# Kernel tuning notes

Hardware: AMD Instinct MI355X
Metric: run time of the kernel (lower is better)

## Reference

```python
import jax, jax.numpy as jnp
import numpy as np

B, T, N = 32, 128, 30
D_T, D_V, D_I = 512, 512, 512


def setup_inputs() -> dict:
    key = jax.random.key(0)
    ks = jax.random.split(key, 9)
    return {
        "h_s": jax.random.normal(ks[0], (B, N, D_T), dtype=jnp.float32),
        "h_v": jax.random.normal(ks[1], (B, T, D_V), dtype=jnp.float32),
        "lengths": jax.random.randint(ks[2], (B,), 1, N + 1, dtype=jnp.int32),
        "W_S": jax.random.normal(ks[3], (D_T, D_I), dtype=jnp.float32) * 0.05,
        "b_S": jax.random.normal(ks[4], (D_I,), dtype=jnp.float32) * 0.05,
        "W_V": jax.random.normal(ks[5], (D_V, D_I), dtype=jnp.float32) * 0.05,
        "b_V": jax.random.normal(ks[6], (D_I,), dtype=jnp.float32) * 0.05,
        "W_w": jax.random.normal(ks[7], (D_I,), dtype=jnp.float32) * 0.05,
        "b_w": jax.random.normal(ks[8], (1,), dtype=jnp.float32) * 0.05,
    }


def reference(h_s, h_v, lengths, W_S, b_S, W_V, b_V, W_w, b_w):
    n_tok = h_s.shape[1]
    # token mask (B, N): 1 where position < length
    mask = (lengths[:, None] >= jnp.arange(1, n_tok + 1)[None, :]).astype(h_s.dtype)
    # loop-invariant projections computed once (the torch loop recomputes per t)
    S = h_s @ W_S + b_S                      # (B, N, D_I)
    V = h_v @ W_V + b_V                      # (B, T, D_I)
    # additive attention scores beta: (B, T, N)
    e = jnp.tanh(S[:, None, :, :] + V[:, :, None, :])  # (B, T, N, D_I)
    beta = jnp.einsum('btnd,d->btn', e, W_w) + b_w[0]
    # masked softmax (non-memory-efficient variant, faithful to source)
    m = mask[:, None, :]                      # (B, 1, N)
    p = jax.nn.softmax(beta * m, axis=-1) * m
    alpha = p / (p.sum(axis=-1, keepdims=True) + 1e-13) + 1e-13  # (B, T, N)
    # attended textual features: (B, T, D_T)
    return jnp.einsum('btn,bnd->btd', alpha, h_s)
```

## Files before the change

kernel.cpp:

```cpp
#include <hip/hip_runtime.h>
#include <math.h>

#define BB 32
#define TT 128
#define NTOK 30
#define DD 512
#define C2F 2.885390081777927f

typedef unsigned short ushortT;
typedef __attribute__((ext_vector_type(8))) short bf16x8;
typedef __attribute__((ext_vector_type(4))) float f32x4;

__device__ __forceinline__ ushortT f2bf(float f) {
    unsigned u = __builtin_bit_cast(unsigned, f);
    u += 0x7fffu + ((u >> 16) & 1u);
    return (ushortT)(u >> 16);
}

__device__ __forceinline__ void load_lds16(const ushortT* g, ushortT* l) {
    __builtin_amdgcn_global_load_lds(
        (const __attribute__((address_space(1))) unsigned int*)g,
        (__attribute__((address_space(3))) unsigned int*)l,
        16, 0, 0);
}

#define NCONV ((BB*NTOK*DD + BB*TT*DD)/4/256)
__global__ __launch_bounds__(256) void prep(
    const float* __restrict__ h_s, const float* __restrict__ h_v,
    const float* __restrict__ W_S, const float* __restrict__ W_V,
    ushortT* __restrict__ Abf_s, ushortT* __restrict__ Abf_v,
    ushortT* __restrict__ WtS, ushortT* __restrict__ WtV)
{
    __shared__ ushortT tile[32][33];
    int bx = blockIdx.x;
    if (bx < NCONV) {
        int i = bx * 256 + threadIdx.x;
        const int n0_4 = BB * NTOK * DD / 4;
        const float* x; ushortT* y;
        if (i < n0_4) { x = h_s; y = Abf_s; }
        else { i -= n0_4; x = h_v; y = Abf_v; }
        float4 v = ((const float4*)x)[i];
        ushort4 o;
        o.x = f2bf(v.x); o.y = f2bf(v.y); o.z = f2bf(v.z); o.w = f2bf(v.w);
        ((ushort4*)y)[i] = o;
        return;
    }
    int idx = bx - NCONV;
    const float* W = (idx & 256) ? W_V : W_S;
    ushortT*    T  = (idx & 256) ? WtV : WtS;
    idx &= 255;
    int k0 = (idx >> 4) * 32, n0 = (idx & 15) * 32;
    int c = threadIdx.x & 31, r8 = threadIdx.x >> 5;
    #pragma unroll
    for (int q = 0; q < 4; ++q) {
        int k = r8 + q * 8;
        tile[k][c] = f2bf(W[(size_t)(k0 + k) * DD + n0 + c]);
    }
    __syncthreads();
    #pragma unroll
    for (int q = 0; q < 4; ++q) {
        int n = r8 + q * 8;
        T[(size_t)(n0 + n) * DD + k0 + c] = tile[c][n];
    }
}

__global__ __launch_bounds__(256) void gemm_mfma(
    const ushortT* __restrict__ Abf_s, const ushortT* __restrict__ Abf_v,
    const ushortT* __restrict__ WtS, const ushortT* __restrict__ WtV,
    const float* __restrict__ b_S, const float* __restrict__ b_V,
    float* __restrict__ Sbuf, float* __restrict__ Vbuf)
{
    __shared__ ushortT ldsA[64 * 64];
    __shared__ ushortT ldsB[64 * 64];
    const ushortT* A; const ushortT* Bt; const float* bias; float* Y; int bm;
    if (blockIdx.x < 15) { A = Abf_s; Bt = WtS; bias = b_S; Y = Sbuf; bm = blockIdx.x * 64; }
    else                 { A = Abf_v; Bt = WtV; bias = b_V; Y = Vbuf; bm = (blockIdx.x - 15) * 64; }

    const int tid  = threadIdx.x;
    const int lane = tid & 63;
    const int wid  = tid >> 6;
    const int wr = wid >> 1, wc = wid & 1;
    const int bn = blockIdx.y * 64;

    const int idx0 = tid,       row0 = idx0 >> 3, ch0 = (idx0 & 7) ^ (row0 & 7);
    const int idx1 = 256 + tid, row1 = idx1 >> 3, ch1 = (idx1 & 7) ^ (row1 & 7);
    const ushortT* gA0 = A  + (size_t)(bm + row0) * DD + ch0 * 8;
    const ushortT* gA1 = A  + (size_t)(bm + row1) * DD + ch1 * 8;
    const ushortT* gB0 = Bt + (size_t)(bn + row0) * DD + ch0 * 8;
    const ushortT* gB1 = Bt + (size_t)(bn + row1) * DD + ch1 * 8;
    ushortT* lA0 = ldsA + wid * 512;
    ushortT* lA1 = ldsA + 2048 + wid * 512;
    ushortT* lB0 = ldsB + wid * 512;
    ushortT* lB1 = ldsB + 2048 + wid * 512;

    const int arow = wr * 32 + (lane & 15);
    const int brow = wc * 32 + (lane & 15);
    const int kq   = lane >> 4;
    const int sw   = lane & 7;

    f32x4 acc[2][2];
    #pragma unroll
    for (int i = 0; i < 2; ++i)
        #pragma unroll
        for (int j = 0; j < 2; ++j)
            acc[i][j] = (f32x4){0.f, 0.f, 0.f, 0.f};

    for (int k0 = 0; k0 < DD; k0 += 64) {
        __syncthreads();
        load_lds16(gA0 + k0, lA0);
        load_lds16(gA1 + k0, lA1);
        load_lds16(gB0 + k0, lB0);
        load_lds16(gB1 + k0, lB1);
        __syncthreads();

        bf16x8 af[2][2], bfr[2][2];
        #pragma unroll
        for (int i = 0; i < 2; ++i)
            #pragma unroll
            for (int s = 0; s < 2; ++s) {
                int ra = arow + i * 16;
                af[i][s]  = *(const bf16x8*)(ldsA + ra * 64 + ((s * 4 + kq) ^ sw) * 8);
                int rb = brow + i * 16;
                bfr[i][s] = *(const bf16x8*)(ldsB + rb * 64 + ((s * 4 + kq) ^ sw) * 8);
            }
        #pragma unroll
        for (int s = 0; s < 2; ++s)
            #pragma unroll
            for (int i = 0; i < 2; ++i)
                #pragma unroll
                for (int j = 0; j < 2; ++j)
                    acc[i][j] = __builtin_amdgcn_mfma_f32_16x16x32_bf16(
                        af[i][s], bfr[j][s], acc[i][j], 0, 0, 0);
    }

    #pragma unroll
    for (int i = 0; i < 2; ++i)
        #pragma unroll
        for (int j = 0; j < 2; ++j) {
            int r = bm + wr * 32 + i * 16 + (lane >> 4) * 4;
            int c = bn + wc * 32 + j * 16 + (lane & 15);
            float bv = bias[c];
            #pragma unroll
            for (int reg = 0; reg < 4; ++reg)
                Y[(size_t)(r + reg) * DD + c] = (acc[i][j][reg] + bv) * C2F;
        }
}

__global__ __launch_bounds__(512) void attend2(
    const float* __restrict__ Sbuf, const float* __restrict__ Vbuf,
    const float* __restrict__ h_s, const int* __restrict__ lengths,
    const float* __restrict__ W_w, const float* __restrict__ b_w,
    float* __restrict__ out)
{
    __shared__ float Slds[NTOK * DD];
    const int b  = blockIdx.x >> 3;
    const int tc = blockIdx.x & 7;
    const int tid = threadIdx.x;
    const int t  = tid >> 5;
    const int dg = tid & 31;
    const int t_glob = tc * 16 + t;
    const int len = lengths[b];
    const float bwv = b_w[0];

    const float4* sSrc = (const float4*)(Sbuf + (size_t)b * NTOK * DD);
    float4* sDst = (float4*)Slds;
    #pragma unroll
    for (int i = 0; i < 8; ++i) {
        int idx = i * 512 + tid;
        if (idx < NTOK * DD / 4) sDst[idx] = sSrc[idx];
    }

    const float* Vrow = Vbuf + ((size_t)(b * TT + t_glob)) * DD;
    float4 v4[4], w4[4];
    #pragma unroll
    for (int c = 0; c < 4; ++c) {
        v4[c] = *(const float4*)&Vrow[dg * 4 + 128 * c];
        w4[c] = *(const float4*)&W_w[dg * 4 + 128 * c];
    }
    float wsum = 0.f;
    #pragma unroll
    for (int c = 0; c < 4; ++c) wsum += w4[c].x + w4[c].y + w4[c].z + w4[c].w;

    __syncthreads();

    float pacc[NTOK];
    #pragma unroll
    for (int n = 0; n < NTOK; ++n) {
        const float* Sr = Slds + n * DD;
        float a = 0.f;
        #pragma unroll
        for (int c = 0; c < 4; ++c) {
            float4 s4 = *(const float4*)&Sr[dg * 4 + 128 * c];
            a = fmaf(w4[c].x, __builtin_amdgcn_rcpf(1.f + __builtin_amdgcn_exp2f(s4.x + v4[c].x)), a);
            a = fmaf(w4[c].y, __builtin_amdgcn_rcpf(1.f + __builtin_amdgcn_exp2f(s4.y + v4[c].y)), a);
            a = fmaf(w4[c].z, __builtin_amdgcn_rcpf(1.f + __builtin_amdgcn_exp2f(s4.z + v4[c].z)), a);
            a = fmaf(w4[c].w, __builtin_amdgcn_rcpf(1.f + __builtin_amdgcn_exp2f(s4.w + v4[c].w)), a);
        }
        pacc[n] = a;
    }
    __syncthreads();

    #pragma unroll
    for (int off = 1; off <= 16; off <<= 1) {
        wsum += __shfl_xor(wsum, off, 64);
        #pragma unroll
        for (int n = 0; n < NTOK; ++n) pacc[n] += __shfl_xor(pacc[n], off, 64);
    }

    float mx = -1e30f;
    #pragma unroll
    for (int n = 0; n < NTOK; ++n) {
        float bn = wsum + bwv - 2.f * pacc[n];
        pacc[n] = bn;
        if (n < len) mx = fmaxf(mx, bn);
    }
    float ssum = 0.f;
    #pragma unroll
    for (int n = 0; n < NTOK; ++n) {
        float e = (n < len) ? __expf(pacc[n] - mx) : 0.f;
        pacc[n] = e;
        ssum += e;
    }
    const float inv = 1.f / (ssum + 1e-13f);
    #pragma unroll
    for (int n = 0; n < NTOK; ++n) pacc[n] = pacc[n] * inv + 1e-13f;

    const float4* hSrc = (const float4*)(h_s + (size_t)b * NTOK * DD);
    #pragma unroll
    for (int i = 0; i < 8; ++i) {
        int idx = i * 512 + tid;
        if (idx < NTOK * DD / 4) sDst[idx] = hSrc[idx];
    }
    __syncthreads();

    float4 acc[4];
    #pragma unroll
    for (int c = 0; c < 4; ++c) acc[c] = make_float4(0.f, 0.f, 0.f, 0.f);
    #pragma unroll
    for (int n = 0; n < NTOK; ++n) {
        float a = pacc[n];
        #pragma unroll
        for (int c = 0; c < 4; ++c) {
            float4 h = *(const float4*)&Slds[n * DD + dg * 4 + 128 * c];
            acc[c].x = fmaf(a, h.x, acc[c].x);
            acc[c].y = fmaf(a, h.y, acc[c].y);
            acc[c].z = fmaf(a, h.z, acc[c].z);
            acc[c].w = fmaf(a, h.w, acc[c].w);
        }
    }
    float* Or = out + ((size_t)(b * TT + t_glob)) * DD;
    #pragma unroll
    for (int c = 0; c < 4; ++c)
        *(float4*)&Or[dg * 4 + 128 * c] = acc[c];
}

extern "C" void kernel_launch(void* const* d_in, const int* in_sizes, int n_in,
                              void* d_out, int out_size, void* d_ws, size_t ws_size,
                              hipStream_t stream) {
    const float* h_s     = (const float*)d_in[0];
    const float* h_v     = (const float*)d_in[1];
    const int*   lengths = (const int*)  d_in[2];
    const float* W_S     = (const float*)d_in[3];
    const float* b_S     = (const float*)d_in[4];
    const float* W_V     = (const float*)d_in[5];
    const float* b_V     = (const float*)d_in[6];
    const float* W_w     = (const float*)d_in[7];
    const float* b_w     = (const float*)d_in[8];
    float* out = (float*)d_out;

    float*   Sbuf  = (float*)d_ws;
    float*   Vbuf  = Sbuf + (size_t)BB * NTOK * DD;
    ushortT* Abf_s = (ushortT*)(Vbuf + (size_t)BB * TT * DD);
    ushortT* Abf_v = Abf_s + (size_t)BB * NTOK * DD;
    ushortT* WtS   = Abf_v + (size_t)BB * TT * DD;
    ushortT* WtV   = WtS + (size_t)DD * DD;

    prep<<<NCONV + 512, 256, 0, stream>>>(h_s, h_v, W_S, W_V, Abf_s, Abf_v, WtS, WtV);
    gemm_mfma<<<dim3(15 + 64, DD / 64), 256, 0, stream>>>(
        Abf_s, Abf_v, WtS, WtV, b_S, b_V, Sbuf, Vbuf);
    attend2<<<BB * 8, 512, 0, stream>>>(Sbuf, Vbuf, h_s, lengths, W_w, b_w, out);
}
```

Baseline: 44.17 us.

## Fuse activation bf16 conversion into GEMM and store projections in bf16

```diff
diff --git a/kernel.cpp b/kernel.cpp
--- a/kernel.cpp
+++ b/kernel.cpp
@@ -7,47 +7,50 @@
 #define DD 512
 #define C2F 2.885390081777927f
 
-typedef unsigned short ushortT;
+typedef unsigned short u16;
 typedef __attribute__((ext_vector_type(8))) short bf16x8;
+typedef __attribute__((ext_vector_type(8))) unsigned short u16x8;
 typedef __attribute__((ext_vector_type(4))) float f32x4;
 
-__device__ __forceinline__ ushortT f2bf(float f) {
+__device__ __forceinline__ u16 f2bf(float f) {
     unsigned u = __builtin_bit_cast(unsigned, f);
     u += 0x7fffu + ((u >> 16) & 1u);
-    return (ushortT)(u >> 16);
-}
-
-__device__ __forceinline__ void load_lds16(const ushortT* g, ushortT* l) {
+    return (u16)(u >> 16);
+}
+__device__ __forceinline__ float bf2f(u16 u) {
+    return __builtin_bit_cast(float, (unsigned)u << 16);
+}
+
+__device__ __forceinline__ void load_lds16(const u16* g, u16* l) {
     __builtin_amdgcn_global_load_lds(
         (const __attribute__((address_space(1))) unsigned int*)g,
         (__attribute__((address_space(3))) unsigned int*)l,
         16, 0, 0);
 }
 
-#define NCONV ((BB*NTOK*DD + BB*TT*DD)/4/256)
+template<int CTRL>
+__device__ __forceinline__ float dpp_add(float x) {
+    int yi = __builtin_amdgcn_update_dpp(0, __builtin_bit_cast(int, x), CTRL, 0xF, 0xF, true);
+    return x + __builtin_bit_cast(float, yi);
+}
+__device__ __forceinline__ float red64(float x) {
+    x = dpp_add<0xB1>(x);
+    x = dpp_add<0x4E>(x);
+    x = dpp_add<0x141>(x);
+    x = dpp_add<0x140>(x);
+    x += __shfl_xor(x, 16, 64);
+    x += __shfl_xor(x, 32, 64);
+    return x;
+}
+
 __global__ __launch_bounds__(256) void prep(
-    const float* __restrict__ h_s, const float* __restrict__ h_v,
     const float* __restrict__ W_S, const float* __restrict__ W_V,
-    ushortT* __restrict__ Abf_s, ushortT* __restrict__ Abf_v,
-    ushortT* __restrict__ WtS, ushortT* __restrict__ WtV)
+    u16* __restrict__ WtS, u16* __restrict__ WtV)
 {
-    __shared__ ushortT tile[32][33];
-    int bx = blockIdx.x;
-    if (bx < NCONV) {
-        int i = bx * 256 + threadIdx.x;
-        const int n0_4 = BB * NTOK * DD / 4;
-        const float* x; ushortT* y;
-        if (i < n0_4) { x = h_s; y = Abf_s; }
-        else { i -= n0_4; x = h_v; y = Abf_v; }
-        float4 v = ((const float4*)x)[i];
-        ushort4 o;
-        o.x = f2bf(v.x); o.y = f2bf(v.y); o.z = f2bf(v.z); o.w = f2bf(v.w);
-        ((ushort4*)y)[i] = o;
-        return;
-    }
-    int idx = bx - NCONV;
+    __shared__ u16 tile[32][33];
+    int idx = blockIdx.x;
     const float* W = (idx & 256) ? W_V : W_S;
-    ushortT*    T  = (idx & 256) ? WtV : WtS;
+    u16*        T  = (idx & 256) ? WtV : WtS;
     idx &= 255;
     int k0 = (idx >> 4) * 32, n0 = (idx & 15) * 32;
     int c = threadIdx.x & 31, r8 = threadIdx.x >> 5;
@@ -65,33 +68,39 @@
 }
 
 __global__ __launch_bounds__(256) void gemm_mfma(
-    const ushortT* __restrict__ Abf_s, const ushortT* __restrict__ Abf_v,
-    const ushortT* __restrict__ WtS, const ushortT* __restrict__ WtV,
+    const float* __restrict__ h_s, const float* __restrict__ h_v,
+    const u16* __restrict__ WtS, const u16* __restrict__ WtV,
     const float* __restrict__ b_S, const float* __restrict__ b_V,
-    float* __restrict__ Sbuf, float* __restrict__ Vbuf)
+    u16* __restrict__ Sbf, u16* __restrict__ Vbf)
 {
-    __shared__ ushortT ldsA[64 * 64];
-    __shared__ ushortT ldsB[64 * 64];
-    const ushortT* A; const ushortT* Bt; const float* bias; float* Y; int bm;
-    if (blockIdx.x < 15) { A = Abf_s; Bt = WtS; bias = b_S; Y = Sbuf; bm = blockIdx.x * 64; }
-    else                 { A = Abf_v; Bt = WtV; bias = b_V; Y = Vbuf; bm = (blockIdx.x - 15) * 64; }
+    __shared__ u16 ldsA[64 * 64];
+    __shared__ u16 ldsB[64 * 64];
+    const int bid = blockIdx.x;
+    const int by  = bid & 7;
+    const int bxx = bid >> 3;
+    const float* A; const u16* Bt; const float* bias; u16* Y; int bm;
+    if (bxx < 15) { A = h_s; Bt = WtS; bias = b_S; Y = Sbf; bm = bxx * 64; }
+    else          { A = h_v; Bt = WtV; bias = b_V; Y = Vbf; bm = (bxx - 15) * 64; }
+    const int bn = by * 64;
 
     const int tid  = threadIdx.x;
     const int lane = tid & 63;
     const int wid  = tid >> 6;
     const int wr = wid >> 1, wc = wid & 1;
-    const int bn = blockIdx.y * 64;
-
-    const int idx0 = tid,       row0 = idx0 >> 3, ch0 = (idx0 & 7) ^ (row0 & 7);
-    const int idx1 = 256 + tid, row1 = idx1 >> 3, ch1 = (idx1 & 7) ^ (row1 & 7);
-    const ushortT* gA0 = A  + (size_t)(bm + row0) * DD + ch0 * 8;
-    const ushortT* gA1 = A  + (size_t)(bm + row1) * DD + ch1 * 8;
-    const ushortT* gB0 = Bt + (size_t)(bn + row0) * DD + ch0 * 8;
-    const ushortT* gB1 = Bt + (size_t)(bn + row1) * DD + ch1 * 8;
-    ushortT* lA0 = ldsA + wid * 512;
-    ushortT* lA1 = ldsA + 2048 + wid * 512;
-    ushortT* lB0 = ldsB + wid * 512;
-    ushortT* lB1 = ldsB + 2048 + wid * 512;
+
+    const int rowA0 = tid >> 3,          chA0 = tid & 7;
+    const int rowA1 = (tid + 256) >> 3,  chA1 = tid & 7;
+    const float* gA0 = A + (size_t)(bm + rowA0) * DD + chA0 * 8;
+    const float* gA1 = A + (size_t)(bm + rowA1) * DD + chA1 * 8;
+    u16* wA0 = ldsA + rowA0 * 64 + ((chA0 ^ (rowA0 & 7)) * 8);
+    u16* wA1 = ldsA + rowA1 * 64 + ((chA1 ^ (rowA1 & 7)) * 8);
+
+    const int idx0 = tid,       rowB0 = idx0 >> 3, chB0 = (idx0 & 7) ^ (rowB0 & 7);
+    const int idx1 = 256 + tid, rowB1 = idx1 >> 3, chB1 = (idx1 & 7) ^ (rowB1 & 7);
+    const u16* gB0 = Bt + (size_t)(bn + rowB0) * DD + chB0 * 8;
+    const u16* gB1 = Bt + (size_t)(bn + rowB1) * DD + chB1 * 8;
+    u16* lB0 = ldsB + wid * 512;
+    u16* lB1 = ldsB + 2048 + wid * 512;
 
     const int arow = wr * 32 + (lane & 15);
     const int brow = wc * 32 + (lane & 15);
@@ -106,9 +115,18 @@
             acc[i][j] = (f32x4){0.f, 0.f, 0.f, 0.f};
 
     for (int k0 = 0; k0 < DD; k0 += 64) {
+        float4 a00 = *(const float4*)(gA0 + k0);
+        float4 a01 = *(const float4*)(gA0 + k0 + 4);
+        float4 a10 = *(const float4*)(gA1 + k0);
+        float4 a11 = *(const float4*)(gA1 + k0 + 4);
         __syncthreads();
-        load_lds16(gA0 + k0, lA0);
-        load_lds16(gA1 + k0, lA1);
+        bf16x8 p0, p1;
+        p0[0]=(short)f2bf(a00.x); p0[1]=(short)f2bf(a00.y); p0[2]=(short)f2bf(a00.z); p0[3]=(short)f2bf(a00.w);
+        p0[4]=(short)f2bf(a01.x); p0[5]=(short)f2bf(a01.y); p0[6]=(short)f2bf(a01.z); p0[7]=(short)f2bf(a01.w);
+        p1[0]=(short)f2bf(a10.x); p1[1]=(short)f2bf(a10.y); p1[2]=(short)f2bf(a10.z); p1[3]=(short)f2bf(a10.w);
+        p1[4]=(short)f2bf(a11.x); p1[5]=(short)f2bf(a11.y); p1[6]=(short)f2bf(a11.z); p1[7]=(short)f2bf(a11.w);
+        *(bf16x8*)wA0 = p0;
+        *(bf16x8*)wA1 = p1;
         load_lds16(gB0 + k0, lB0);
         load_lds16(gB1 + k0, lB1);
         __syncthreads();
@@ -142,75 +160,72 @@
             float bv = bias[c];
             #pragma unroll
             for (int reg = 0; reg < 4; ++reg)
-                Y[(size_t)(r + reg) * DD + c] = (acc[i][j][reg] + bv) * C2F;
-        }
-}
-
-__global__ __launch_bounds__(512) void attend2(
-    const float* __restrict__ Sbuf, const float* __restrict__ Vbuf,
+                Y[(size_t)(r + reg) * DD + c] = f2bf((acc[i][j][reg] + bv) * C2F);
+        }
+}
+
+__global__ __launch_bounds__(512) void attend3(
+    const u16* __restrict__ Sbf, const u16* __restrict__ Vbf,
     const float* __restrict__ h_s, const int* __restrict__ lengths,
     const float* __restrict__ W_w, const float* __restrict__ b_w,
     float* __restrict__ out)
 {
-    __shared__ float Slds[NTOK * DD];
-    const int b  = blockIdx.x >> 3;
-    const int tc = blockIdx.x & 7;
-    const int tid = threadIdx.x;
-    const int t  = tid >> 5;
-    const int dg = tid & 31;
-    const int t_glob = tc * 16 + t;
+    __shared__ u16 Slds[NTOK * DD];
+    const int b  = blockIdx.x >> 4;
+    const int tc = blockIdx.x & 15;
+    const int tid  = threadIdx.x;
+    const int w    = tid >> 6;
+    const int lane = tid & 63;
+    const int t_glob = tc * 8 + w;
     const int len = lengths[b];
+    const int d0 = lane * 8;
     const float bwv = b_w[0];
 
-    const float4* sSrc = (const float4*)(Sbuf + (size_t)b * NTOK * DD);
-    float4* sDst = (float4*)Slds;
-    #pragma unroll
-    for (int i = 0; i < 8; ++i) {
-        int idx = i * 512 + tid;
-        if (idx < NTOK * DD / 4) sDst[idx] = sSrc[idx];
-    }
-
-    const float* Vrow = Vbuf + ((size_t)(b * TT + t_glob)) * DD;
-    float4 v4[4], w4[4];
-    #pragma unroll
-    for (int c = 0; c < 4; ++c) {
-        v4[c] = *(const float4*)&Vrow[dg * 4 + 128 * c];
-        w4[c] = *(const float4*)&W_w[dg * 4 + 128 * c];
-    }
-    float wsum = 0.f;
-    #pragma unroll
-    for (int c = 0; c < 4; ++c) wsum += w4[c].x + w4[c].y + w4[c].z + w4[c].w;
+    {
+        const uint4* src = (const uint4*)(Sbf + (size_t)b * NTOK * DD);
+        uint4* dst = (uint4*)Slds;
+        #pragma unroll
+        for (int i = 0; i < 4; ++i) {
+            int idx = i * 512 + tid;
+            if (idx < NTOK * DD / 8) dst[idx] = src[idx];
+        }
+    }
+
+    float v[8], ww[8];
+    {
+        u16x8 v8 = *(const u16x8*)(Vbf + ((size_t)(b * TT + t_glob)) * DD + d0);
+        float4 w0 = *(const float4*)&W_w[d0];
+        float4 w1 = *(const float4*)&W_w[d0 + 4];
+        #pragma unroll
+        for (int j = 0; j < 8; ++j) v[j] = bf2f(v8[j]);
+        ww[0]=w0.x; ww[1]=w0.y; ww[2]=w0.z; ww[3]=w0.w;
+        ww[4]=w1.x; ww[5]=w1.y; ww[6]=w1.z; ww[7]=w1.w;
+    }
+    float wpart = 0.f;
+    #pragma unroll
+    for (int j = 0; j < 8; ++j) wpart += ww[j];
+    const float wsum = red64(wpart);
 
     __syncthreads();
 
     float pacc[NTOK];
     #pragma unroll
     for (int n = 0; n < NTOK; ++n) {
-        const float* Sr = Slds + n * DD;
+        u16x8 s8 = *(const u16x8*)(Slds + n * DD + d0);
         float a = 0.f;
         #pragma unroll
-        for (int c = 0; c < 4; ++c) {
-            float4 s4 = *(const float4*)&Sr[dg * 4 + 128 * c];
-            a = fmaf(w4[c].x, __builtin_amdgcn_rcpf(1.f + __builtin_amdgcn_exp2f(s4.x + v4[c].x)), a);
-            a = fmaf(w4[c].y, __builtin_amdgcn_rcpf(1.f + __builtin_amdgcn_exp2f(s4.y + v4[c].y)), a);
-            a = fmaf(w4[c].z, __builtin_amdgcn_rcpf(1.f + __builtin_amdgcn_exp2f(s4.z + v4[c].z)), a);
-            a = fmaf(w4[c].w, __builtin_amdgcn_rcpf(1.f + __builtin_amdgcn_exp2f(s4.w + v4[c].w)), a);
-        }
-        pacc[n] = a;
-    }
-    __syncthreads();
-
-    #pragma unroll
-    for (int off = 1; off <= 16; off <<= 1) {
-        wsum += __shfl_xor(wsum, off, 64);
-        #pragma unroll
-        for (int n = 0; n < NTOK; ++n) pacc[n] += __shfl_xor(pacc[n], off, 64);
-    }
+        for (int j = 0; j < 8; ++j) {
+            float e = __builtin_amdgcn_exp2f(bf2f(s8[j]) + v[j]);
+            a = fmaf(ww[j], __builtin_amdgcn_rcpf(1.f + e), a);
+        }
+        pacc[n] = red64(a);
+    }
+    __syncthreads();
 
     float mx = -1e30f;
     #pragma unroll
     for (int n = 0; n < NTOK; ++n) {
-        float bn = wsum + bwv - 2.f * pacc[n];
+        float bn = fmaf(-2.f, pacc[n], wsum + bwv);
         pacc[n] = bn;
         if (n < len) mx = fmaxf(mx, bn);
     }
@@ -223,35 +238,37 @@
     }
     const float inv = 1.f / (ssum + 1e-13f);
     #pragma unroll
-    for (int n = 0; n < NTOK; ++n) pacc[n] = pacc[n] * inv + 1e-13f;
-
-    const float4* hSrc = (const float4*)(h_s + (size_t)b * NTOK * DD);
-    #pragma unroll
-    for (int i = 0; i < 8; ++i) {
-        int idx = i * 512 + tid;
-        if (idx < NTOK * DD / 4) sDst[idx] = hSrc[idx];
-    }
-    __syncthreads();
-
-    float4 acc[4];
-    #pragma unroll
-    for (int c = 0; c < 4; ++c) acc[c] = make_float4(0.f, 0.f, 0.f, 0.f);
+    for (int n = 0; n < NTOK; ++n) pacc[n] = fmaf(pacc[n], inv, 1e-13f);
+
+    {
+        const float4* src = (const float4*)(h_s + (size_t)b * NTOK * DD);
+        ushort4* dst = (ushort4*)Slds;
+        #pragma unroll
+        for (int i = 0; i < 8; ++i) {
+            int idx = i * 512 + tid;
+            if (idx < NTOK * DD / 4) {
+                float4 hv = src[idx];
+                ushort4 pk;
+                pk.x = f2bf(hv.x); pk.y = f2bf(hv.y);
+                pk.z = f2bf(hv.z); pk.w = f2bf(hv.w);
+                dst[idx] = pk;
+            }
+        }
+    }
+    __syncthreads();
+
+    float acc8[8] = {};
     #pragma unroll
     for (int n = 0; n < NTOK; ++n) {
         float a = pacc[n];
-        #pragma unroll
-        for (int c = 0; c < 4; ++c) {
-            float4 h = *(const float4*)&Slds[n * DD + dg * 4 + 128 * c];
-            acc[c].x = fmaf(a, h.x, acc[c].x);
-            acc[c].y = fmaf(a, h.y, acc[c].y);
-            acc[c].z = fmaf(a, h.z, acc[c].z);
-            acc[c].w = fmaf(a, h.w, acc[c].w);
-        }
-    }
-    float* Or = out + ((size_t)(b * TT + t_glob)) * DD;
-    #pragma unroll
-    for (int c = 0; c < 4; ++c)
-        *(float4*)&Or[dg * 4 + 128 * c] = acc[c];
+        u16x8 h8 = *(const u16x8*)(Slds + n * DD + d0);
+        #pragma unroll
+        for (int j = 0; j < 8; ++j)
+            acc8[j] = fmaf(a, bf2f(h8[j]), acc8[j]);
+    }
+    float* Or = out + ((size_t)(b * TT + t_glob)) * DD + d0;
+    *(float4*)&Or[0] = make_float4(acc8[0], acc8[1], acc8[2], acc8[3]);
+    *(float4*)&Or[4] = make_float4(acc8[4], acc8[5], acc8[6], acc8[7]);
 }
 
 extern "C" void kernel_launch(void* const* d_in, const int* in_sizes, int n_in,
@@ -268,15 +285,13 @@
     const float* b_w     = (const float*)d_in[8];
     float* out = (float*)d_out;
 
-    float*   Sbuf  = (float*)d_ws;
-    float*   Vbuf  = Sbuf + (size_t)BB * NTOK * DD;
-    ushortT* Abf_s = (ushortT*)(Vbuf + (size_t)BB * TT * DD);
-    ushortT* Abf_v = Abf_s + (size_t)BB * NTOK * DD;
-    ushortT* WtS   = Abf_v + (size_t)BB * TT * DD;
-    ushortT* WtV   = WtS + (size_t)DD * DD;
-
-    prep<<<NCONV + 512, 256, 0, stream>>>(h_s, h_v, W_S, W_V, Abf_s, Abf_v, WtS, WtV);
-    gemm_mfma<<<dim3(15 + 64, DD / 64), 256, 0, stream>>>(
-        Abf_s, Abf_v, WtS, WtV, b_S, b_V, Sbuf, Vbuf);
-    attend2<<<BB * 8, 512, 0, stream>>>(Sbuf, Vbuf, h_s, lengths, W_w, b_w, out);
-}
+    u16* Sbf = (u16*)d_ws;
+    u16* Vbf = Sbf + (size_t)BB * NTOK * DD;
+    u16* WtS = Vbf + (size_t)BB * TT * DD;
+    u16* WtV = WtS + (size_t)DD * DD;
+
+    prep<<<512, 256, 0, stream>>>(W_S, W_V, WtS, WtV);
+    gemm_mfma<<<(15 + 64) * 8, 256, 0, stream>>>(
+        h_s, h_v, WtS, WtV, b_S, b_V, Sbf, Vbf);
+    attend3<<<BB * 16, 512, 0, stream>>>(Sbf, Vbf, h_s, lengths, W_w, b_w, out);
+}
```

Result: slower. 50.63 us (+14.6%).
